# Kernel tuning notes

Measured on AMD Instinct MI355X. Metric: run time of the kernel, lower is better.

## Reference

```python
import jax, jax.numpy as jnp
import numpy as np

B, LQ, LK = 4, 1024, 2048
DQ, DK, DV, D = 1024, 512, 512, 1024
H = 16
HD = D // H
EPS = 1e-5


def setup_inputs() -> dict:
    key = jax.random.key(0)
    ks = jax.random.split(key, 12)
    s = lambda fan: 1.0 / np.sqrt(fan)
    return {
        "query": jax.random.normal(ks[0], (B, LQ, DQ), jnp.float32),
        "key": jax.random.normal(ks[1], (B, LK, DK), jnp.float32),
        "value": jax.random.normal(ks[2], (B, LK, DV), jnp.float32),
        "key_padding_mask": jnp.ones((B, LK), jnp.int32),
        "Wq": jax.random.normal(ks[3], (DQ, D), jnp.float32) * s(DQ),
        "bq": jnp.zeros((D,), jnp.float32),
        "Wk": jax.random.normal(ks[4], (DK, D), jnp.float32) * s(DK),
        "bk": jnp.zeros((D,), jnp.float32),
        "Wv": jax.random.normal(ks[5], (DV, D), jnp.float32) * s(DV),
        "bv": jnp.zeros((D,), jnp.float32),
        "Wo": jax.random.normal(ks[6], (D, D), jnp.float32) * s(D),
        "bo": jnp.zeros((D,), jnp.float32),
        "ln_g": jnp.ones((D,), jnp.float32),
        "ln_b": jnp.zeros((D,), jnp.float32),
    }


def _layer_norm(x, g, b):
    mu = jnp.mean(x, axis=-1, keepdims=True)
    var = jnp.mean(jnp.square(x - mu), axis=-1, keepdims=True)
    return (x - mu) * jax.lax.rsqrt(var + EPS) * g + b


def reference(query, key, value, key_padding_mask, Wq, bq, Wk, bk, Wv, bv, Wo, bo, ln_g, ln_b):
    residual = query
    qn = _layer_norm(query, ln_g, ln_b)
    # projections -> [B, L, H, HD]
    q = (qn @ Wq + bq).reshape(B, LQ, H, HD)
    k = (key @ Wk + bk).reshape(B, LK, H, HD)
    v = (value @ Wv + bv).reshape(B, LK, H, HD)
    scale = HD ** -0.5
    # scores [B, H, Lq, Lk]
    scores = jnp.einsum("bqhd,bkhd->bhqk", q, k) * scale
    mask = (key_padding_mask != 0)[:, None, None, :]  # True = keep
    scores = jnp.where(mask, scores, -jnp.inf)
    attn = jax.nn.softmax(scores, axis=-1)
    # dropout is identity in eval mode
    ctx = jnp.einsum("bhqk,bkhd->bqhd", attn, v).reshape(B, LQ, D)
    out = ctx @ Wo + bo
    return out + residual
```

## Files before the change

kernel.cpp:

```cpp
#include <hip/hip_runtime.h>
#include <hip/hip_bf16.h>
#include <stdint.h>

#define Bn 4
#define LQ 1024
#define LK 2048
#define Dm 1024
#define Hn 16
#define HD 64

typedef __attribute__((ext_vector_type(4))) float f32x4;
typedef __attribute__((ext_vector_type(16))) float f32x16;
typedef __attribute__((ext_vector_type(8))) short bf16x8;

__device__ __forceinline__ ushort f2bf(float f) {
  union { float f; uint32_t u; } v; v.f = f;
  uint32_t r = v.u + 0x7FFF + ((v.u >> 16) & 1);
  return (ushort)(r >> 16);
}

__device__ __forceinline__ uint32_t cvt_pk_bf16(float lo, float hi) {
  uint32_t r;
  asm("v_cvt_pk_bf16_f32 %0, %1, %2" : "=v"(r) : "v"(lo), "v"(hi));
  return r;
}

__device__ __forceinline__ float exp2v(float x) {
  float r;
  asm("v_exp_f32 %0, %1" : "=v"(r) : "v"(x));
  return r;
}

__device__ __forceinline__ void gload16(const void* g, void* lds) {
  __builtin_amdgcn_global_load_lds(
      (const __attribute__((address_space(1))) void*)g,
      (__attribute__((address_space(3))) void*)lds, 16, 0, 0);
}

__device__ __forceinline__ void wait_vm0_barrier() {
  asm volatile("s_waitcnt vmcnt(0)" ::: "memory");
  __builtin_amdgcn_s_barrier();
}

__device__ __forceinline__ void wait_all_barrier() {
  asm volatile("s_waitcnt vmcnt(0) lgkmcnt(0)" ::: "memory");
  __builtin_amdgcn_s_barrier();
}

__device__ __forceinline__ void wait_lgkm0_barrier() {
  asm volatile("s_waitcnt lgkmcnt(0)" ::: "memory");
  __builtin_amdgcn_s_barrier();
}

__global__ __launch_bounds__(256) void transpose4_kernel(
    const float* __restrict__ Wq, ushort* __restrict__ WqT,
    const float* __restrict__ Wk, ushort* __restrict__ WkT,
    const float* __restrict__ Wv, ushort* __restrict__ WvT,
    const float* __restrict__ Wo, ushort* __restrict__ WoT) {
  __shared__ float tile[64][65];
  int id = blockIdx.x;
  const float* W; ushort* Wt; int K, N, kx, ny;
  if (id < 256)      { W = Wq; Wt = WqT; K = 1024; N = 1024; kx = id & 15; ny = id >> 4; }
  else if (id < 384) { int i = id - 256; W = Wk; Wt = WkT; K = 512; N = 1024; kx = i & 7; ny = i >> 3; }
  else if (id < 512) { int i = id - 384; W = Wv; Wt = WvT; K = 512; N = 1024; kx = i & 7; ny = i >> 3; }
  else               { int i = id - 512; W = Wo; Wt = WoT; K = 1024; N = 1024; kx = i & 15; ny = i >> 4; }
  int k0 = kx * 64, n0 = ny * 64;
  int tx = threadIdx.x & 63, ty = threadIdx.x >> 6;
#pragma unroll
  for (int i = 0; i < 16; ++i) {
    int r = ty + i * 4;
    tile[r][tx] = W[(size_t)(k0 + r) * N + n0 + tx];
  }
  __syncthreads();
#pragma unroll
  for (int i = 0; i < 16; ++i) {
    int r = ty + i * 4;
    Wt[(size_t)(n0 + r) * K + k0 + tx] = f2bf(tile[tx][r]);
  }
}

__global__ __launch_bounds__(256) void cast2_kernel(
    const float4* __restrict__ k4, ushort4* __restrict__ kb,
    const float4* __restrict__ v4, ushort4* __restrict__ vb) {
  const int n4 = (8192 * 512) / 4;
  int i = blockIdx.x * 256 + threadIdx.x;
  int stride = gridDim.x * 256;
  for (; i < 2 * n4; i += stride) {
    float4 v = (i < n4) ? k4[i] : v4[i - n4];
    ushort4 o = make_ushort4(f2bf(v.x), f2bf(v.y), f2bf(v.z), f2bf(v.w));
    if (i < n4) kb[i] = o; else vb[i - n4] = o;
  }
}

__global__ __launch_bounds__(256) void ln_kernel(
    const float* __restrict__ x, const float* __restrict__ g,
    const float* __restrict__ b, ushort* __restrict__ y) {
  int row = blockIdx.x;
  const float4* xr = (const float4*)(x + (size_t)row * 1024);
  float4 v = xr[threadIdx.x];
  float s1 = v.x + v.y + v.z + v.w;
  float s2 = v.x * v.x + v.y * v.y + v.z * v.z + v.w * v.w;
#pragma unroll
  for (int off = 32; off > 0; off >>= 1) {
    s1 += __shfl_down(s1, off);
    s2 += __shfl_down(s2, off);
  }
  __shared__ float r1[4], r2[4];
  int w = threadIdx.x >> 6, lane = threadIdx.x & 63;
  if (lane == 0) { r1[w] = s1; r2[w] = s2; }
  __syncthreads();
  s1 = r1[0] + r1[1] + r1[2] + r1[3];
  s2 = r2[0] + r2[1] + r2[2] + r2[3];
  float mu = s1 * (1.0f / 1024.0f);
  float var = s2 * (1.0f / 1024.0f) - mu * mu;
  float rstd = rsqrtf(var + 1e-5f);
  float4 gv = ((const float4*)g)[threadIdx.x];
  float4 bv = ((const float4*)b)[threadIdx.x];
  ushort4 o;
  o.x = f2bf((v.x - mu) * rstd * gv.x + bv.x);
  o.y = f2bf((v.y - mu) * rstd * gv.y + bv.y);
  o.z = f2bf((v.z - mu) * rstd * gv.z + bv.z);
  o.w = f2bf((v.w - mu) * rstd * gv.w + bv.w);
  ((ushort4*)(y + (size_t)row * 1024))[threadIdx.x] = o;
}

__global__ __launch_bounds__(512) void qkv_gemm_kernel(
    const ushort* __restrict__ qn, const ushort* __restrict__ WqT,
    const float* __restrict__ bq, ushort* __restrict__ Qb,
    const ushort* __restrict__ keyb, const ushort* __restrict__ WkT,
    const float* __restrict__ bk, ushort* __restrict__ Kb,
    const ushort* __restrict__ valb, const ushort* __restrict__ WvT,
    const float* __restrict__ bv, ushort* __restrict__ Vt, float qscale) {
  __shared__ ushort As[2][128 * 64];
  __shared__ ushort Bs[2][128 * 64];

  int o = blockIdx.x;
  int logical = (o & 7) * 160 + (o >> 3);
  int g5 = logical / 5, r5 = logical % 5;
  const ushort* A; const ushort* Bt; const float* bias; ushort* out;
  int K, bx, by, epi; float osc = 1.0f;
  if (r5 == 0) {
    A = qn; Bt = WqT; bias = bq; out = Qb; K = 1024; epi = 0;
    osc = qscale; bx = g5 & 7; by = g5 >> 3;
  } else if (r5 <= 2) {
    int i = g5 * 2 + (r5 - 1);
    A = keyb; Bt = WkT; bias = bk; out = Kb; K = 512; epi = 0;
    bx = i & 7; by = i >> 3;
  } else {
    int i = g5 * 2 + (r5 - 3);
    A = valb; Bt = WvT; bias = bv; out = Vt; K = 512; epi = 1;
    bx = i & 7; by = i >> 3;
  }
  const int N = 1024;
  const int m0 = by * 128, n0 = bx * 128;

  const int t = threadIdx.x;
  const int lane = t & 63;
  const int w = t >> 6;
  const int wm = w >> 2, wn = w & 3;
  const int l31 = lane & 31, hl = lane >> 5;

  f32x16 acc[2] = {};

  const ushort* Ap[2];
  const ushort* Bp[2];
#pragma unroll
  for (int i = 0; i < 2; ++i) {
    int c = t + i * 512;
    int r = c >> 3, x = ((c & 7) ^ (r & 7)) * 8;
    Ap[i] = A + (size_t)(m0 + r) * K + x;
    Bp[i] = Bt + (size_t)(n0 + r) * K + x;
  }

  auto stage = [&](int buf, int kt) {
    gload16(Ap[0] + kt, (char*)As[buf] + (size_t)t * 16);
    gload16(Ap[1] + kt, (char*)As[buf] + (size_t)(t + 512) * 16);
    gload16(Bp[0] + kt, (char*)Bs[buf] + (size_t)t * 16);
    gload16(Bp[1] + kt, (char*)Bs[buf] + (size_t)(t + 512) * 16);
  };

  stage(0, 0);

  int cur = 0;
  for (int kt = 0; kt < K; kt += 64) {
    if (kt + 64 < K) {
      stage(cur ^ 1, kt + 64);
      asm volatile("s_waitcnt vmcnt(4)" ::: "memory");
    } else {
      asm volatile("s_waitcnt vmcnt(0)" ::: "memory");
    }
    __builtin_amdgcn_s_barrier();

    bf16x8 af[2][4], bfr[4];
#pragma unroll
    for (int m = 0; m < 2; ++m) {
      int row = wm * 64 + m * 32 + l31;
      const char* ar = (const char*)As[cur] + row * 128;
      int rs = row & 7;
#pragma unroll
      for (int kc = 0; kc < 4; ++kc)
        af[m][kc] = *(const bf16x8*)(ar + ((kc * 2 + hl) ^ rs) * 16);
    }
    {
      int row = wn * 32 + l31;
      const char* br = (const char*)Bs[cur] + row * 128;
      int rs = row & 7;
#pragma unroll
      for (int kc = 0; kc < 4; ++kc)
        bfr[kc] = *(const bf16x8*)(br + ((kc * 2 + hl) ^ rs) * 16);
    }
#pragma unroll
    for (int kc = 0; kc < 4; ++kc)
#pragma unroll
      for (int m = 0; m < 2; ++m)
        acc[m] = __builtin_amdgcn_mfma_f32_32x32x16_bf16(af[m][kc], bfr[kc], acc[m], 0, 0, 0);

    wait_lgkm0_barrier();
    cur ^= 1;
  }

  const int col = n0 + wn * 32 + l31;
  const float bias_v = bias[col];

#pragma unroll
  for (int m = 0; m < 2; ++m) {
    int rbase = m0 + wm * 64 + m * 32 + hl * 4;
#pragma unroll
    for (int rq = 0; rq < 4; ++rq) {
      int row0 = rbase + rq * 8;
      if (epi == 1) {
        int bb = row0 >> 11;
        int key = row0 & 2047;
        int h = col >> 6, hd = col & 63;
        ushort4 pk;
        pk.x = f2bf(acc[m][rq * 4 + 0] + bias_v);
        pk.y = f2bf(acc[m][rq * 4 + 1] + bias_v);
        pk.z = f2bf(acc[m][rq * 4 + 2] + bias_v);
        pk.w = f2bf(acc[m][rq * 4 + 3] + bias_v);
        *(ushort4*)(out + ((size_t)((bb * 16 + h) * 64 + hd)) * 2048 + key) = pk;
      } else {
#pragma unroll
        for (int j = 0; j < 4; ++j) {
          int row = row0 + j;
          float v = (acc[m][rq * 4 + j] + bias_v) * osc;
          out[(size_t)row * N + col] = f2bf(v);
        }
      }
    }
  }
}

__global__ __launch_bounds__(512) void oproj_gemm_kernel(
    const ushort* __restrict__ A, const ushort* __restrict__ Bt,
    const float* __restrict__ bias, float* __restrict__ Cout,
    const float* __restrict__ residual, int M, int N, int K) {
  __shared__ ushort As[2][128 * 64];
  __shared__ ushort Bs[2][128 * 64];
  const int t = threadIdx.x;
  const int lane = t & 63;
  const int w = t >> 6;
  const int wm = w >> 2, wn = w & 3;
  const int m0 = blockIdx.y * 128, n0 = blockIdx.x * 128;
  const int l31 = lane & 31, hl = lane >> 5;

  f32x16 acc[2] = {};

  const ushort* Ap[2];
  const ushort* Bp[2];
#pragma unroll
  for (int i = 0; i < 2; ++i) {
    int c = t + i * 512;
    int r = c >> 3, x = ((c & 7) ^ (r & 7)) * 8;
    Ap[i] = A + (size_t)(m0 + r) * K + x;
    Bp[i] = Bt + (size_t)(n0 + r) * K + x;
  }

  auto stage = [&](int buf, int kt) {
    gload16(Ap[0] + kt, (char*)As[buf] + (size_t)t * 16);
    gload16(Ap[1] + kt, (char*)As[buf] + (size_t)(t + 512) * 16);
    gload16(Bp[0] + kt, (char*)Bs[buf] + (size_t)t * 16);
    gload16(Bp[1] + kt, (char*)Bs[buf] + (size_t)(t + 512) * 16);
  };

  stage(0, 0);

  int cur = 0;
  for (int kt = 0; kt < K; kt += 64) {
    if (kt + 64 < K) {
      stage(cur ^ 1, kt + 64);
      asm volatile("s_waitcnt vmcnt(4)" ::: "memory");
    } else {
      asm volatile("s_waitcnt vmcnt(0)" ::: "memory");
    }
    __builtin_amdgcn_s_barrier();

    bf16x8 af[2][4], bfr[4];
#pragma unroll
    for (int m = 0; m < 2; ++m) {
      int row = wm * 64 + m * 32 + l31;
      const char* ar = (const char*)As[cur] + row * 128;
      int rs = row & 7;
#pragma unroll
      for (int kc = 0; kc < 4; ++kc)
        af[m][kc] = *(const bf16x8*)(ar + ((kc * 2 + hl) ^ rs) * 16);
    }
    {
      int row = wn * 32 + l31;
      const char* br = (const char*)Bs[cur] + row * 128;
      int rs = row & 7;
#pragma unroll
      for (int kc = 0; kc < 4; ++kc)
        bfr[kc] = *(const bf16x8*)(br + ((kc * 2 + hl) ^ rs) * 16);
    }
#pragma unroll
    for (int kc = 0; kc < 4; ++kc)
#pragma unroll
      for (int m = 0; m < 2; ++m)
        acc[m] = __builtin_amdgcn_mfma_f32_32x32x16_bf16(af[m][kc], bfr[kc], acc[m], 0, 0, 0);

    wait_lgkm0_barrier();
    cur ^= 1;
  }

  const int col = n0 + wn * 32 + l31;
  const float bias_v = bias[col];

#pragma unroll
  for (int m = 0; m < 2; ++m) {
    int rbase = m0 + wm * 64 + m * 32 + hl * 4;
#pragma unroll
    for (int rq = 0; rq < 4; ++rq) {
      int row0 = rbase + rq * 8;
#pragma unroll
      for (int j = 0; j < 4; ++j) {
        size_t idx = (size_t)(row0 + j) * N + col;
        Cout[idx] = acc[m][rq * 4 + j] + bias_v + residual[idx];
      }
    }
  }
}

__global__ __launch_bounds__(256) void attn_kernel(
    const ushort* __restrict__ Qb, const ushort* __restrict__ Kb,
    const ushort* __restrict__ Vt, const int* __restrict__ mask,
    ushort* __restrict__ ctx) {
  __shared__ __align__(16) char smem[128 + 2 * 16384];
  int* tilevalid = (int*)smem;
  char* KsBase = smem + 128;

  const int t = threadIdx.x, lane = t & 63, w = t >> 6;
  const int l31 = lane & 31, hl = lane >> 5;
  int o = blockIdx.x;
  int logical = (o & 7) * 64 + (o >> 3);
  const int b = logical >> 7;
  const int hh = (logical >> 3) & 15;
  const int q0 = (logical & 7) * 128;
  const int* maskp = mask + b * 2048;

  const int cA = t, cB = t + 256;
  const int rA = cA >> 3, rB = cB >> 3;
  const int xA = ((cA & 7) ^ (rA & 7)) * 8, xB = ((cB & 7) ^ (rB & 7)) * 8;
  const ushort* kpA = Kb + ((size_t)(b * 2048 + rA)) * 1024 + hh * 64 + xA;
  const ushort* kpB = Kb + ((size_t)(b * 2048 + rB)) * 1024 + hh * 64 + xB;
  const ushort* vpA = Vt + ((size_t)((b * 16 + hh) * 64 + rA)) * 2048 + xA;
  const ushort* vpB = Vt + ((size_t)((b * 16 + hh) * 64 + rB)) * 2048 + xB;

  auto stageKV = [&](int buf) {
    char* kd = KsBase + buf * 8192;
    char* vd = KsBase + 16384 + buf * 8192;
    gload16(kpA, kd + cA * 16);
    gload16(kpB, kd + cB * 16);
    gload16(vpA, vd + cA * 16);
    gload16(vpB, vd + cB * 16);
  };

  if (t < 32) tilevalid[t] = 1;
  __syncthreads();
  stageKV(0);
  {
    const int* mp = maskp + t * 8;
    int ok = 1;
#pragma unroll
    for (int j = 0; j < 8; ++j) ok &= (mp[j] != 0) ? 1 : 0;
    atomicAnd(&tilevalid[t >> 3], ok);
  }

  bf16x8 qf[4];
  {
    int qrow = q0 + w * 32 + l31;
    const ushort* qp = Qb + ((size_t)(b * 1024 + qrow)) * 1024 + hh * 64 + hl * 8;
    qf[0] = *(const bf16x8*)(qp);
    qf[1] = *(const bf16x8*)(qp + 16);
    qf[2] = *(const bf16x8*)(qp + 32);
    qf[3] = *(const bf16x8*)(qp + 48);
  }

  const int rs = l31 & 7;
  int lo[2][2][4];
#pragma unroll
  for (int bu = 0; bu < 2; ++bu)
#pragma unroll
    for (int r2 = 0; r2 < 2; ++r2)
#pragma unroll
      for (int kc = 0; kc < 4; ++kc)
        lo[bu][r2][kc] = 128 + bu * 8192 + (r2 * 32 + l31) * 128 + (((kc * 2 + hl) ^ rs) * 16);

  f32x16 o_acc[2] = {};
  float l_run = 0.0f;
  const float FOFF = 16.0f;

  wait_all_barrier();

  auto body = [&](const int CUR, int TILE) __attribute__((always_inline)) {
    if (TILE + 1 < 32) {
      kpA += 64 * 1024; kpB += 64 * 1024; vpA += 64; vpB += 64;
      stageKV(CUR ^ 1);
    }

    f32x16 sacc[2] = {};
    __builtin_amdgcn_s_setprio(1);
#pragma unroll
    for (int kb = 0; kb < 2; ++kb)
#pragma unroll
      for (int kc = 0; kc < 4; ++kc) {
        bf16x8 kf = *(const bf16x8*)(smem + lo[CUR][kb][kc]);
        sacc[kb] = __builtin_amdgcn_mfma_f32_32x32x16_bf16(kf, qf[kc], sacc[kb], 0, 0, 0);
      }
    __builtin_amdgcn_s_setprio(0);

    int allv = __builtin_amdgcn_readfirstlane(tilevalid[TILE]);
    if (!allv) {
      const int* mrow = maskp + TILE * 64 + 4 * hl;
#pragma unroll
      for (int kb = 0; kb < 2; ++kb)
#pragma unroll
        for (int rq = 0; rq < 4; ++rq) {
          int4 mv = *(const int4*)(mrow + kb * 32 + rq * 8);
          sacc[kb][rq * 4 + 0] = mv.x ? sacc[kb][rq * 4 + 0] : -1e30f;
          sacc[kb][rq * 4 + 1] = mv.y ? sacc[kb][rq * 4 + 1] : -1e30f;
          sacc[kb][rq * 4 + 2] = mv.z ? sacc[kb][rq * 4 + 2] : -1e30f;
          sacc[kb][rq * 4 + 3] = mv.w ? sacc[kb][rq * 4 + 3] : -1e30f;
        }
    }

    float psA = 0.0f, psB = 0.0f;
    uint32_t cpk[2][8];
#pragma unroll
    for (int kb = 0; kb < 2; ++kb)
#pragma unroll
      for (int rr = 0; rr < 8; ++rr) {
        float pa = exp2v(sacc[kb][2 * rr] - FOFF);
        float pb = exp2v(sacc[kb][2 * rr + 1] - FOFF);
        psA += pa; psB += pb;
        cpk[kb][rr] = cvt_pk_bf16(pa, pb);
      }
    float psum = psA + psB;
    {
      float s1 = psum, s2 = psum;
      asm("v_permlane32_swap_b32 %0, %1" : "+v"(s1), "+v"(s2));
      psum += hl ? s1 : s2;
    }
    l_run += psum;

    __builtin_amdgcn_s_setprio(1);
#pragma unroll
    for (int ks = 0; ks < 4; ++ks) {
      const int kb = ks >> 1, ci = (ks & 1) * 4;
      uint32_t a0 = cpk[kb][ci],     b0 = cpk[kb][ci + 2];
      uint32_t a1 = cpk[kb][ci + 1], b1 = cpk[kb][ci + 3];
      asm("v_permlane32_swap_b32 %0, %1" : "+v"(a0), "+v"(b0));
      asm("v_permlane32_swap_b32 %0, %1" : "+v"(a1), "+v"(b1));
      union { uint32_t u[4]; bf16x8 v; } pb_;
      pb_.u[0] = a0; pb_.u[1] = a1; pb_.u[2] = b0; pb_.u[3] = b1;
#pragma unroll
      for (int df = 0; df < 2; ++df) {
        bf16x8 vf = *(const bf16x8*)(smem + lo[CUR][df][ks] + 16384);
        o_acc[df] = __builtin_amdgcn_mfma_f32_32x32x16_bf16(vf, pb_.v, o_acc[df], 0, 0, 0);
      }
    }
    __builtin_amdgcn_s_setprio(0);

    wait_vm0_barrier();
  };

  for (int tile = 0; tile < 32; tile += 2) {
    body(0, tile);
    body(1, tile + 1);
  }

  float inv = l_run > 0.0f ? 1.0f / l_run : 0.0f;
  char* ob = KsBase + w * 4096;
#pragma unroll
  for (int df = 0; df < 2; ++df)
#pragma unroll
    for (int rq = 0; rq < 4; ++rq) {
      ushort4 pk;
      pk.x = f2bf(o_acc[df][rq * 4 + 0] * inv);
      pk.y = f2bf(o_acc[df][rq * 4 + 1] * inv);
      pk.z = f2bf(o_acc[df][rq * 4 + 2] * inv);
      pk.w = f2bf(o_acc[df][rq * 4 + 3] * inv);
      *(ushort4*)(ob + l31 * 128 + (((df * 4 + rq) ^ (l31 & 7)) * 16) + hl * 8) = pk;
    }
  asm volatile("s_waitcnt lgkmcnt(0)" ::: "memory");
#pragma unroll
  for (int i = 0; i < 4; ++i) {
    int q = (lane >> 3) + i * 8;
    int ch = lane & 7;
    uint4 v = *(const uint4*)(ob + q * 128 + ((ch ^ (q & 7)) * 16));
    int qrow = q0 + w * 32 + q;
    *(uint4*)(ctx + ((size_t)(b * 1024 + qrow)) * 1024 + hh * 64 + ch * 8) = v;
  }
}

extern "C" void kernel_launch(void* const* d_in, const int* in_sizes, int n_in,
                              void* d_out, int out_size, void* d_ws, size_t ws_size,
                              hipStream_t stream) {
  const float* query = (const float*)d_in[0];
  const float* key   = (const float*)d_in[1];
  const float* value = (const float*)d_in[2];
  const int*   mask  = (const int*)d_in[3];
  const float* Wq = (const float*)d_in[4];
  const float* bq = (const float*)d_in[5];
  const float* Wk = (const float*)d_in[6];
  const float* bk = (const float*)d_in[7];
  const float* Wv = (const float*)d_in[8];
  const float* bv = (const float*)d_in[9];
  const float* Wo = (const float*)d_in[10];
  const float* bo = (const float*)d_in[11];
  const float* ln_g = (const float*)d_in[12];
  const float* ln_b = (const float*)d_in[13];
  float* out = (float*)d_out;

  char* p = (char*)d_ws;
  auto alloc = [&](size_t elems) { ushort* r = (ushort*)p; p += elems * 2; return r; };
  ushort* WqT  = alloc((size_t)1024 * 1024);
  ushort* WkT  = alloc((size_t)1024 * 512);
  ushort* WvT  = alloc((size_t)1024 * 512);
  ushort* WoT  = alloc((size_t)1024 * 1024);
  ushort* qn   = alloc((size_t)4096 * 1024);
  ushort* keyb = alloc((size_t)8192 * 512);
  ushort* valb = alloc((size_t)8192 * 512);
  ushort* Qb   = alloc((size_t)4096 * 1024);
  ushort* Kb   = alloc((size_t)8192 * 1024);
  ushort* Vt   = alloc((size_t)8192 * 1024);
  ushort* ctx  = alloc((size_t)4096 * 1024);
  (void)ws_size; (void)in_sizes; (void)n_in; (void)out_size;

  const float QSCALE = 0.125f * 1.44269504f;

  dim3 blk(256);
  dim3 blk5(512);
  transpose4_kernel<<<dim3(768), blk, 0, stream>>>(Wq, WqT, Wk, WkT, Wv, WvT, Wo, WoT);
  cast2_kernel<<<dim3(2048), blk, 0, stream>>>(
      (const float4*)key, (ushort4*)keyb, (const float4*)value, (ushort4*)valb);
  ln_kernel<<<dim3(4096), blk, 0, stream>>>(query, ln_g, ln_b, qn);

  qkv_gemm_kernel<<<dim3(1280), blk5, 0, stream>>>(
      qn, WqT, bq, Qb, keyb, WkT, bk, Kb, valb, WvT, bv, Vt, QSCALE);

  attn_kernel<<<dim3(512), blk, 0, stream>>>(Qb, Kb, Vt, mask, ctx);

  oproj_gemm_kernel<<<dim3(8, 32), blk5, 0, stream>>>(ctx, WoT, bo, out, query, 4096, 1024, 1024);
}
```

Before: 141.9 us.

## Triple-buffer K/V tiles in attention kernel with two-tile prefetch depth

Moves the attention kernel's K/V staging from double to triple buffering, so two tiles are prefetched ahead using per-tile offsets instead of advancing pointers. Each iteration now waits with a partial vmcnt and a barrier at the top, rather than a full vmcnt(0) plus barrier at the end, so more global-to-LDS traffic can overlap compute. The cost is 16KB more LDS per block, which may reduce occupancy, and a subtler wait/barrier ordering.

```diff
diff --git a/kernel.cpp b/kernel.cpp
--- a/kernel.cpp
+++ b/kernel.cpp
@@ -35,16 +35,6 @@
   __builtin_amdgcn_global_load_lds(
       (const __attribute__((address_space(1))) void*)g,
       (__attribute__((address_space(3))) void*)lds, 16, 0, 0);
-}
-
-__device__ __forceinline__ void wait_vm0_barrier() {
-  asm volatile("s_waitcnt vmcnt(0)" ::: "memory");
-  __builtin_amdgcn_s_barrier();
-}
-
-__device__ __forceinline__ void wait_all_barrier() {
-  asm volatile("s_waitcnt vmcnt(0) lgkmcnt(0)" ::: "memory");
-  __builtin_amdgcn_s_barrier();
 }
 
 __device__ __forceinline__ void wait_lgkm0_barrier() {
@@ -344,9 +334,10 @@
     const ushort* __restrict__ Qb, const ushort* __restrict__ Kb,
     const ushort* __restrict__ Vt, const int* __restrict__ mask,
     ushort* __restrict__ ctx) {
-  __shared__ __align__(16) char smem[128 + 2 * 16384];
+  __shared__ __align__(16) char smem[128 + 3 * 16384];
   int* tilevalid = (int*)smem;
   char* KsBase = smem + 128;
+  char* VsBase = smem + 128 + 24576;
 
   const int t = threadIdx.x, lane = t & 63, w = t >> 6;
   const int l31 = lane & 31, hl = lane >> 5;
@@ -365,18 +356,21 @@
   const ushort* vpA = Vt + ((size_t)((b * 16 + hh) * 64 + rA)) * 2048 + xA;
   const ushort* vpB = Vt + ((size_t)((b * 16 + hh) * 64 + rB)) * 2048 + xB;
 
-  auto stageKV = [&](int buf) {
+  auto stageKV = [&](int buf, int tile) {
     char* kd = KsBase + buf * 8192;
-    char* vd = KsBase + 16384 + buf * 8192;
-    gload16(kpA, kd + cA * 16);
-    gload16(kpB, kd + cB * 16);
-    gload16(vpA, vd + cA * 16);
-    gload16(vpB, vd + cB * 16);
+    char* vd = VsBase + buf * 8192;
+    size_t ko = (size_t)tile * 65536;
+    size_t vo = (size_t)tile * 64;
+    gload16(kpA + ko, kd + cA * 16);
+    gload16(kpB + ko, kd + cB * 16);
+    gload16(vpA + vo, vd + cA * 16);
+    gload16(vpB + vo, vd + cB * 16);
   };
 
   if (t < 32) tilevalid[t] = 1;
   __syncthreads();
-  stageKV(0);
+  stageKV(0, 0);
+  stageKV(1, 1);
   {
     const int* mp = maskp + t * 8;
     int ok = 1;
@@ -396,9 +390,9 @@
   }
 
   const int rs = l31 & 7;
-  int lo[2][2][4];
-#pragma unroll
-  for (int bu = 0; bu < 2; ++bu)
+  int lo[3][2][4];
+#pragma unroll
+  for (int bu = 0; bu < 3; ++bu)
 #pragma unroll
     for (int r2 = 0; r2 < 2; ++r2)
 #pragma unroll
@@ -409,13 +403,17 @@
   float l_run = 0.0f;
   const float FOFF = 16.0f;
 
-  wait_all_barrier();
-
-  auto body = [&](const int CUR, int TILE) __attribute__((always_inline)) {
-    if (TILE + 1 < 32) {
-      kpA += 64 * 1024; kpB += 64 * 1024; vpA += 64; vpB += 64;
-      stageKV(CUR ^ 1);
-    }
+  asm volatile("s_waitcnt lgkmcnt(0)" ::: "memory");
+  __builtin_amdgcn_s_barrier();
+
+  auto body = [&](const int CUR, int TILE, const int LAST) __attribute__((always_inline)) {
+    if (LAST) {
+      asm volatile("s_waitcnt vmcnt(0)" ::: "memory");
+    } else {
+      asm volatile("s_waitcnt vmcnt(4)" ::: "memory");
+    }
+    __builtin_amdgcn_s_barrier();
+    if (TILE + 2 < 32) stageKV((CUR + 2) % 3, TILE + 2);
 
     f32x16 sacc[2] = {};
     __builtin_amdgcn_s_setprio(1);
@@ -474,20 +472,22 @@
       pb_.u[0] = a0; pb_.u[1] = a1; pb_.u[2] = b0; pb_.u[3] = b1;
 #pragma unroll
       for (int df = 0; df < 2; ++df) {
-        bf16x8 vf = *(const bf16x8*)(smem + lo[CUR][df][ks] + 16384);
+        bf16x8 vf = *(const bf16x8*)(smem + lo[CUR][df][ks] + 24576);
         o_acc[df] = __builtin_amdgcn_mfma_f32_32x32x16_bf16(vf, pb_.v, o_acc[df], 0, 0, 0);
       }
     }
     __builtin_amdgcn_s_setprio(0);
-
-    wait_vm0_barrier();
   };
 
-  for (int tile = 0; tile < 32; tile += 2) {
-    body(0, tile);
-    body(1, tile + 1);
-  }
-
+  for (int t3 = 0; t3 < 30; t3 += 3) {
+    body(0, t3, 0);
+    body(1, t3 + 1, 0);
+    body(2, t3 + 2, 0);
+  }
+  body(0, 30, 0);
+  body(1, 31, 1);
+
+  __builtin_amdgcn_s_barrier();
   float inv = l_run > 0.0f ? 1.0f / l_run : 0.0f;
   char* ob = KsBase + w * 4096;
 #pragma unroll
```

Result: no change. 140.1 us (-1.3%).
